# Kernel tuning notes

Hardware: AMD Instinct MI355X
Metric: run time of the kernel (lower is better)

The kernel has to match this reference:

```python
import jax, jax.numpy as jnp
import numpy as np

HIDDEN = 3072
N_HEADS = 24
N_KV = 8
HEAD_DIM = HIDDEN // N_HEADS          # 128
ROT = int(HEAD_DIM * 0.75)            # 96 (partial rotary)
OP_SIZE = N_HEADS * HEAD_DIM + 2 * N_KV * HEAD_DIM  # 5120
LORA_R = 256
LORA_SCALE = 512.0 / LORA_R           # 2.0
ROPE_THETA = 10000.0
SCALE = HEAD_DIM ** -0.5


def setup_inputs() -> dict:
    key = jax.random.key(0)
    ks = jax.random.split(key, 8)
    B, S = 2, 2048
    hidden_states = jax.random.normal(ks[0], (B, S, HIDDEN), dtype=jnp.float32)
    position_ids = jnp.arange(B * S, dtype=jnp.int64 if jax.config.jax_enable_x64 else jnp.int32).reshape(B, S)
    w = lambda k, o, i: jax.random.normal(k, (o, i), dtype=jnp.float32) * (i ** -0.5)
    return {
        "hidden_states": hidden_states,
        "Wqkv": w(ks[1], OP_SIZE, HIDDEN),
        "Aqkv": w(ks[2], LORA_R, HIDDEN),
        "Bqkv": w(ks[3], OP_SIZE, LORA_R) * 0.01,
        "Wo": w(ks[4], HIDDEN, N_HEADS * HEAD_DIM),
        "Ao": w(ks[5], LORA_R, N_HEADS * HEAD_DIM),
        "Bo": w(ks[6], HIDDEN, LORA_R) * 0.01,
        "position_ids": position_ids,
    }


def _lora_linear(x, W, A, Bm):
    # base GEMM + low-rank LoRA update, scaling = alpha/r
    return x @ W.T + (x @ A.T) @ Bm.T * LORA_SCALE


def _rotate_half(x):
    h = x.shape[-1] // 2
    return jnp.concatenate((-x[..., h:], x[..., :h]), axis=-1)


def reference(hidden_states, Wqkv, Aqkv, Bqkv, Wo, Ao, Bo, position_ids):
    B, S, _ = hidden_states.shape
    qkv = _lora_linear(hidden_states, Wqkv, Aqkv, Bqkv)  # [B,S,5120]
    q_pos = N_HEADS * HEAD_DIM
    kv_pos = N_KV * HEAD_DIM
    q = qkv[..., :q_pos].reshape(B, S, N_HEADS, HEAD_DIM)
    k = qkv[..., q_pos:q_pos + kv_pos].reshape(B, S, N_KV, HEAD_DIM)
    v = qkv[..., q_pos + kv_pos:].reshape(B, S, N_KV, HEAD_DIM)

    # partial RoPE: cos/sin cache over rotary_ndims=96
    inv_freq = 1.0 / (ROPE_THETA ** (jnp.arange(0, ROT, 2, dtype=jnp.float32) / ROT))  # [48]
    freqs = position_ids.astype(jnp.float32)[..., None] * inv_freq  # [B,S,48]
    emb = jnp.concatenate((freqs, freqs), axis=-1)                   # [B,S,96]
    cos = jnp.cos(emb)[:, :, None, :]  # broadcast over head axis (bsnd)
    sin = jnp.sin(emb)[:, :, None, :]

    def rope(x):
        xr, xp = x[..., :ROT], x[..., ROT:]
        xr = xr * cos + _rotate_half(xr) * sin
        return jnp.concatenate((xr, xp), axis=-1)

    q = rope(q)
    k = rope(k)

    # GQA: repeat kv heads to match query heads
    groups = N_HEADS // N_KV
    k = jnp.repeat(k, groups, axis=2)
    v = jnp.repeat(v, groups, axis=2)

    scores = jnp.einsum('bqhd,bkhd->bhqk', q, k) * SCALE  # [B,H,S,S]
    causal = jnp.tril(jnp.ones((S, S), dtype=bool))
    scores = jnp.where(causal, scores, jnp.finfo(scores.dtype).min)
    probs = jax.nn.softmax(scores, axis=-1)
    attn = jnp.einsum('bhqk,bkhd->bqhd', probs, v).reshape(B, S, N_HEADS * HEAD_DIM)
    return _lora_linear(attn, Wo, Ao, Bo)
```

## Files before the change

### kernel.cpp

```cpp
#include <hip/hip_runtime.h>

typedef unsigned short u16;
typedef unsigned int   u32;

typedef __bf16 bf16_t;
typedef bf16_t bf16x8 __attribute__((ext_vector_type(8)));
typedef float  f32x4  __attribute__((ext_vector_type(4)));
typedef float  f32x16 __attribute__((ext_vector_type(16)));
typedef u16    u16x8  __attribute__((ext_vector_type(8)));
typedef u32    u32x4  __attribute__((ext_vector_type(4)));

__device__ __forceinline__ float bf2f(u16 u) { return __uint_as_float(((u32)u) << 16); }
__device__ __forceinline__ u16 f2bf(float f) {
  u32 u = __float_as_uint(f);
  u32 r = u + 0x7fffu + ((u >> 16) & 1u);
  return (u16)(r >> 16);
}
__device__ __forceinline__ float fast_exp2(float x) { return __builtin_amdgcn_exp2f(x); }

__device__ __forceinline__ void gload_lds16(const u16* g, u16* l) {
  __builtin_amdgcn_global_load_lds(
      (const __attribute__((address_space(1))) void*)g,
      (__attribute__((address_space(3))) void*)l,
      16, 0, 0);
}

#define SBAR0() __builtin_amdgcn_sched_barrier(0)
#define HWBAR() __builtin_amdgcn_s_barrier()

__global__ void k_cast_str(const float* __restrict__ in, u16* __restrict__ out,
                           int C8, int L, int off, float scale) {
  const int r  = blockIdx.y;
  const int c8 = blockIdx.x * 128 + threadIdx.x;
  if (c8 >= C8) return;
  const f32x4* p = (const f32x4*)(in + (size_t)r * (C8 * 8) + c8 * 8);
  f32x4 a = p[0], b = p[1];
  u16x8 o;
  o[0] = f2bf(a[0] * scale); o[1] = f2bf(a[1] * scale);
  o[2] = f2bf(a[2] * scale); o[3] = f2bf(a[3] * scale);
  o[4] = f2bf(b[0] * scale); o[5] = f2bf(b[1] * scale);
  o[6] = f2bf(b[2] * scale); o[7] = f2bf(b[3] * scale);
  *(u16x8*)(out + (size_t)r * L + off + c8 * 8) = o;
}

__global__ void k_red4_cast(const float* __restrict__ t4, u16* __restrict__ out,
                            int C8, int L, int off, float scale, size_t plane) {
  const int r  = blockIdx.y;
  const int c8 = blockIdx.x * 64 + threadIdx.x;
  if (c8 >= C8) return;
  size_t base = (size_t)r * (C8 * 8) + c8 * 8;
  float s[8];
#pragma unroll
  for (int j = 0; j < 8; ++j) s[j] = 0.f;
#pragma unroll
  for (int p = 0; p < 4; ++p) {
    const f32x4* q = (const f32x4*)(t4 + p * plane + base);
    f32x4 a = q[0], b = q[1];
    s[0] += a[0]; s[1] += a[1]; s[2] += a[2]; s[3] += a[3];
    s[4] += b[0]; s[5] += b[1]; s[6] += b[2]; s[7] += b[3];
  }
  u16x8 o;
#pragma unroll
  for (int j = 0; j < 8; ++j) o[j] = f2bf(s[j] * scale);
  *(u16x8*)(out + (size_t)r * L + off + c8 * 8) = o;
}

__global__ __launch_bounds__(256) void k_gemm_bt_sk(
    const u16* __restrict__ A, const u16* __restrict__ B, float* __restrict__ C,
    int M, int N, int lda, int ldb, int kc) {
  __shared__ u16 As[64][64 + 8];
  __shared__ u16 Bs[64][64 + 8];
  const int tid   = threadIdx.x;
  const int lane  = tid & 63;
  const int w     = tid >> 6;
  const int wm    = (w >> 1) * 32;
  const int wn    = (w & 1) * 32;
  const int row16 = lane & 15;
  const int quad  = lane >> 4;
  const int m0 = blockIdx.y * 64;
  const int n0 = blockIdx.x * 64;
  const int ldr = tid >> 2;
  const int ldc = (tid & 3) * 16;
  const int z   = blockIdx.z;
  float* Cz = C + (size_t)z * M * N;
  const int kbeg = z * kc, kend = kbeg + kc;

  f32x4 acc[2][2] = {};

  for (int k0 = kbeg; k0 < kend; k0 += 64) {
    const u16* ga = A + (size_t)(m0 + ldr) * lda + (k0 + ldc);
    const u16* gb = B + (size_t)(n0 + ldr) * ldb + (k0 + ldc);
    u16x8 a0 = *(const u16x8*)ga;
    u16x8 a1 = *(const u16x8*)(ga + 8);
    u16x8 b0 = *(const u16x8*)gb;
    u16x8 b1 = *(const u16x8*)(gb + 8);
    __syncthreads();
    *(u16x8*)&As[ldr][ldc]     = a0;
    *(u16x8*)&As[ldr][ldc + 8] = a1;
    *(u16x8*)&Bs[ldr][ldc]     = b0;
    *(u16x8*)&Bs[ldr][ldc + 8] = b1;
    __syncthreads();
#pragma unroll
    for (int kk = 0; kk < 64; kk += 32) {
      bf16x8 af0 = *(const bf16x8*)&As[wm + row16][kk + quad * 8];
      bf16x8 af1 = *(const bf16x8*)&As[wm + 16 + row16][kk + quad * 8];
      bf16x8 bg0 = *(const bf16x8*)&Bs[wn + row16][kk + quad * 8];
      bf16x8 bg1 = *(const bf16x8*)&Bs[wn + 16 + row16][kk + quad * 8];
      acc[0][0] = __builtin_amdgcn_mfma_f32_16x16x32_bf16(af0, bg0, acc[0][0], 0, 0, 0);
      acc[0][1] = __builtin_amdgcn_mfma_f32_16x16x32_bf16(af0, bg1, acc[0][1], 0, 0, 0);
      acc[1][0] = __builtin_amdgcn_mfma_f32_16x16x32_bf16(af1, bg0, acc[1][0], 0, 0, 0);
      acc[1][1] = __builtin_amdgcn_mfma_f32_16x16x32_bf16(af1, bg1, acc[1][1], 0, 0, 0);
    }
  }
#pragma unroll
  for (int tm = 0; tm < 2; ++tm)
#pragma unroll
    for (int tn = 0; tn < 2; ++tn) {
      int gm = m0 + wm + tm * 16 + quad * 4;
      int gn = n0 + wn + tn * 16 + row16;
#pragma unroll
      for (int r = 0; r < 4; ++r)
        Cz[(size_t)(gm + r) * N + gn] = acc[tm][tn][r];
    }
}

__device__ __forceinline__ void stage_half(
    int H, int nt4,
    const u16* __restrict__ A, const u16* __restrict__ B, int K,
    int m0, int n0, u16* AsB, u16* BsB,
    int w, int rowin, int colsw) {
  if (H >= nt4) return;
  const int t = H >> 2, slot = H & 3;
  const int half = slot & 1;
  const u16* G = (slot < 2) ? A : B;
  const int r0 = (slot < 2) ? m0 : n0;
  u16* lds = ((slot < 2) ? AsB : BsB) + (t & 1) * 16384 + half * 8192;
  const int k0 = t * 64;
#pragma unroll
  for (int i = 0; i < 2; ++i) {
    const int chunk = w * 2 + i;
    const int row = half * 128 + chunk * 8 + rowin;
    gload_lds16(G + (size_t)(r0 + row) * K + k0 + colsw, lds + chunk * 512);
  }
}

__device__ __forceinline__ bf16x8 frag_ld(const u16* base, int row, int c16) {
  return *(const bf16x8*)(base + row * 64 + ((c16 ^ (row & 7)) << 3));
}

template <int RB>
__device__ __forceinline__ void gemm256_group(
    int k, int nt,
    const u16* __restrict__ A, const u16* __restrict__ B, int K,
    int m0, int n0, u16* AsB, u16* BsB,
    int wr, int wc, int row16, int quad, int w, int rowin, int colsw,
    f32x4 (&acc)[8][4]) {
  const u16* Ab = AsB + RB * 16384;
  const u16* Bb = BsB + RB * 16384;
  const int nt4 = nt * 4;
  bf16x8 a0[4][2], a1[4][2], b0[2][2], b1[2][2];

#pragma unroll
  for (int mf = 0; mf < 4; ++mf)
#pragma unroll
    for (int kk = 0; kk < 2; ++kk)
      a0[mf][kk] = frag_ld(Ab, wr * 128 + mf * 16 + row16, kk * 4 + quad);
#pragma unroll
  for (int nf = 0; nf < 2; ++nf)
#pragma unroll
    for (int kk = 0; kk < 2; ++kk)
      b0[nf][kk] = frag_ld(Bb, wc * 64 + nf * 16 + row16, kk * 4 + quad);
  stage_half(4 * k + 5, nt4, A, B, K, m0, n0, AsB, BsB, w, rowin, colsw);
  SBAR0(); HWBAR(); SBAR0();
  __builtin_amdgcn_s_setprio(1);
#pragma unroll
  for (int mf = 0; mf < 4; ++mf)
#pragma unroll
    for (int nf = 0; nf < 2; ++nf)
#pragma unroll
      for (int kk = 0; kk < 2; ++kk)
        acc[mf][nf] = __builtin_amdgcn_mfma_f32_16x16x32_bf16(a0[mf][kk], b0[nf][kk], acc[mf][nf], 0, 0, 0);
  __builtin_amdgcn_s_setprio(0);
  SBAR0(); HWBAR(); SBAR0();

#pragma unroll
  for (int nf = 0; nf < 2; ++nf)
#pragma unroll
    for (int kk = 0; kk < 2; ++kk)
      b1[nf][kk] = frag_ld(Bb, wc * 64 + 32 + nf * 16 + row16, kk * 4 + quad);
  stage_half(4 * k + 6, nt4, A, B, K, m0, n0, AsB, BsB, w, rowin, colsw);
  SBAR0(); HWBAR(); SBAR0();
  __builtin_amdgcn_s_setprio(1);
#pragma unroll
  for (int mf = 0; mf < 4; ++mf)
#pragma unroll
    for (int nf = 0; nf < 2; ++nf)
#pragma unroll
      for (int kk = 0; kk < 2; ++kk)
        acc[mf][2 + nf] = __builtin_amdgcn_mfma_f32_16x16x32_bf16(a0[mf][kk], b1[nf][kk], acc[mf][2 + nf], 0, 0, 0);
  __builtin_amdgcn_s_setprio(0);
  SBAR0(); HWBAR(); SBAR0();

#pragma unroll
  for (int mf = 0; mf < 4; ++mf)
#pragma unroll
    for (int kk = 0; kk < 2; ++kk)
      a1[mf][kk] = frag_ld(Ab, wr * 128 + 64 + mf * 16 + row16, kk * 4 + quad);
  stage_half(4 * k + 7, nt4, A, B, K, m0, n0, AsB, BsB, w, rowin, colsw);
  SBAR0(); HWBAR(); SBAR0();
  __builtin_amdgcn_s_setprio(1);
#pragma unroll
  for (int mf = 0; mf < 4; ++mf)
#pragma unroll
    for (int nf = 0; nf < 2; ++nf)
#pragma unroll
      for (int kk = 0; kk < 2; ++kk)
        acc[4 + mf][nf] = __builtin_amdgcn_mfma_f32_16x16x32_bf16(a1[mf][kk], b0[nf][kk], acc[4 + mf][nf], 0, 0, 0);
  __builtin_amdgcn_s_setprio(0);
  SBAR0(); HWBAR(); SBAR0();

  stage_half(4 * k + 8, nt4, A, B, K, m0, n0, AsB, BsB, w, rowin, colsw);
  SBAR0();
  if (k < nt - 2) { asm volatile("s_waitcnt vmcnt(2)" ::: "memory"); }
  else            { asm volatile("s_waitcnt vmcnt(0)" ::: "memory"); }
  HWBAR(); SBAR0();
  __builtin_amdgcn_s_setprio(1);
#pragma unroll
  for (int mf = 0; mf < 4; ++mf)
#pragma unroll
    for (int nf = 0; nf < 2; ++nf)
#pragma unroll
      for (int kk = 0; kk < 2; ++kk)
        acc[4 + mf][2 + nf] = __builtin_amdgcn_mfma_f32_16x16x32_bf16(a1[mf][kk], b1[nf][kk], acc[4 + mf][2 + nf], 0, 0, 0);
  __builtin_amdgcn_s_setprio(0);
  SBAR0(); HWBAR(); SBAR0();
}

__global__ __launch_bounds__(512, 2) void k_gemm256(
    const u16* __restrict__ A, const u16* __restrict__ B, float* __restrict__ C,
    int M, int N, int K) {
  __shared__ u16 As[2 * 16384];
  __shared__ u16 Bs[2 * 16384];

  const int tid   = threadIdx.x;
  const int lane  = tid & 63;
  const int w     = tid >> 6;
  const int wr    = w >> 2;
  const int wc    = w & 3;
  const int row16 = lane & 15;
  const int quad  = lane >> 4;
  const int rowin = lane >> 3;
  const int colsw = ((lane & 7) ^ (lane >> 3)) << 3;

  const int nwg = (int)gridDim.x;
  const int bid = (int)blockIdx.x;
  const int xcd = bid & 7, rest = bid >> 3;
  const int qq = nwg >> 3, rr = nwg & 7;
  const int wg = (xcd < rr ? xcd * (qq + 1) : rr * (qq + 1) + (xcd - rr) * qq) + rest;
  const int nbx = N >> 8;
  const int m0 = (wg / nbx) << 8;
  const int n0 = (wg % nbx) << 8;

  const int nt = K >> 6;
  f32x4 acc[8][4] = {};

#pragma unroll
  for (int H = 0; H < 5; ++H)
    stage_half(H, nt * 4, A, B, K, m0, n0, As, Bs, w, rowin, colsw);
  asm volatile("s_waitcnt vmcnt(2)" ::: "memory");
  HWBAR(); SBAR0();

  int k = 0;
  for (; k + 1 < nt; k += 2) {
    gemm256_group<0>(k,     nt, A, B, K, m0, n0, As, Bs, wr, wc, row16, quad, w, rowin, colsw, acc);
    gemm256_group<1>(k + 1, nt, A, B, K, m0, n0, As, Bs, wr, wc, row16, quad, w, rowin, colsw, acc);
  }
  if (k < nt)
    gemm256_group<0>(k, nt, A, B, K, m0, n0, As, Bs, wr, wc, row16, quad, w, rowin, colsw, acc);

#pragma unroll
  for (int mi = 0; mi < 8; ++mi) {
    const int gm = m0 + wr * 128 + mi * 16 + quad * 4;
#pragma unroll
    for (int nj = 0; nj < 4; ++nj) {
      const int gn = n0 + wc * 64 + nj * 16 + row16;
#pragma unroll
      for (int r = 0; r < 4; ++r)
        C[(size_t)(gm + r) * N + gn] = acc[mi][nj][r];
    }
  }
}

__global__ void k_rope_tab(const int* __restrict__ pos_ids, float* __restrict__ tab) {
  const int t = threadIdx.x;
  const int r = blockIdx.x * 4 + t / 48;
  const int j = t % 48;
  const float pos = (float)pos_ids[r];
  float invf = powf(10000.0f, -(float)j * (1.0f / 48.0f));
  float e = pos * invf;
  tab[(size_t)r * 96 + j]      = cosf(e);
  tab[(size_t)r * 96 + 48 + j] = sinf(e);
}

__global__ void k_rope_split(const float* __restrict__ qkv, const float* __restrict__ tab,
                             u16* __restrict__ qb, u16* __restrict__ kb) {
  const int r  = blockIdx.x;
  const int hh = blockIdx.y;
  const int d  = threadIdx.x;
  const float* src;
  if (hh < 24) src = qkv + (size_t)r * 5120 + hh * 128;
  else         src = qkv + (size_t)r * 5120 + 3072 + (hh - 24) * 128;
  float x = src[d];
  float outv;
  if (d >= 96) {
    outv = x;
  } else {
    int j = (d < 48) ? d : d - 48;
    float c  = tab[(size_t)r * 96 + j];
    float sn = tab[(size_t)r * 96 + 48 + j];
    if (d < 48) outv = x * c - src[d + 48] * sn;
    else        outv = x * c + src[d - 48] * sn;
  }
  u16 o = f2bf(outv);
  if (hh < 24) qb[((size_t)r * 24 + hh) * 128 + d] = o;
  else         kb[((size_t)r * 8 + (hh - 24)) * 128 + d] = o;
}

__global__ void k_vtrans(const float* __restrict__ qkv, u16* __restrict__ vtg) {
  const int d  = threadIdx.x;
  const int kg = blockIdx.x;
  const int bk = blockIdx.y;
  const int b = bk >> 3, kvh = bk & 7;
  const float* src = qkv + (size_t)(b * 2048 + kg * 8) * 5120 + 4096 + kvh * 128 + d;
  u16x8 pack;
#pragma unroll
  for (int t = 0; t < 8; ++t) pack[t] = f2bf(src[(size_t)t * 5120]);
  *(u16x8*)(vtg + ((size_t)bk * 128 + d) * 2048 + kg * 8) = pack;
}

__global__ __launch_bounds__(256) void k_attn_mfma(
    const u16* __restrict__ qb, const u16* __restrict__ kb, const u16* __restrict__ vtg,
    u16* __restrict__ attnw) {
  __shared__ u16 KsA[8192], VtA[8192], KsB[8192], VtB[8192];

  const int tid  = threadIdx.x;
  const int lane = tid & 63;
  const int w    = tid >> 6;
  const int l31  = lane & 31;
  const int hi   = lane >> 5;
  const int r7   = lane & 7;
  const int qt   = (int)gridDim.x - 1 - (int)blockIdx.x;
  const int bh   = blockIdx.y;
  const int b    = bh / 24;
  const int h    = bh % 24;
  const int kvh  = h / 3;
  const int q0   = qt * 128;
  const int qrow = q0 + w * 32 + l31;

  const u16* qrb = qb + (((size_t)(b * 2048 + qrow)) * 24 + h) * 128;
  bf16x8 qf[8];
#pragma unroll
  for (int kk = 0; kk < 8; ++kk) qf[kk] = *(const bf16x8*)(qrb + kk * 16 + hi * 8);

  const u16* kbbase = kb + ((size_t)(b * 2048) * 8 + kvh) * 128;
  const u16* vtbase = vtg + (size_t)(b * 8 + kvh) * 128 * 2048;

  f32x16 o32[4] = {};
  float m_st = -INFINITY, l_st = 0.f;
  const float C1 = 0.08838834764831845f * 1.4426950408889634f;
  const int ntile = 2 * qt + 2;

#define STAGE(Kd, Vd, KB0)                                                          \
  {                                                                                 \
    _Pragma("unroll")                                                               \
    for (int i = 0; i < 4; ++i) {                                                   \
      const int c = w * 4 + i;                                                      \
      const int rowk = 4 * c + (lane >> 4);                                         \
      gload_lds16(kbbase + (size_t)((KB0) + rowk) * 1024 +                          \
                      (((lane & 15) ^ (rowk & 7)) << 3),                            \
                  (Kd) + c * 512);                                                  \
      const int rowv = 8 * c + (lane >> 3);                                         \
      gload_lds16(vtbase + (size_t)rowv * 2048 + (KB0) +                            \
                      (((lane & 7) ^ (rowv & 7)) << 3),                             \
                  (Vd) + c * 512);                                                  \
    }                                                                               \
  }

  STAGE(KsA, VtA, 0);
  __syncthreads();

  for (int t = 0; t < ntile; ++t) {
    const int kb0 = t * 64;
    const u16* Kc = (t & 1) ? KsB : KsA;
    const u16* Vc = (t & 1) ? VtB : VtA;
    if (t + 1 < ntile) {
      u16* Kn = (t & 1) ? KsA : KsB;
      u16* Vn = (t & 1) ? VtA : VtB;
      STAGE(Kn, Vn, kb0 + 64);
    }

    f32x16 s[2] = {};
    __builtin_amdgcn_s_setprio(1);
#pragma unroll
    for (int kk = 0; kk < 8; ++kk) {
#pragma unroll
      for (int kt = 0; kt < 2; ++kt) {
        const int row = kt * 32 + l31;
        bf16x8 kf = *(const bf16x8*)&Kc[row * 128 + (((2 * kk + hi) ^ r7) << 3)];
        s[kt] = __builtin_amdgcn_mfma_f32_32x32x16_bf16(kf, qf[kk], s[kt], 0, 0, 0);
      }
    }
    __builtin_amdgcn_s_setprio(0);

    if (kb0 >= q0) {
#pragma unroll
      for (int kt = 0; kt < 2; ++kt)
#pragma unroll
        for (int r = 0; r < 16; ++r) {
          const int key = kb0 + 32 * kt + (r & 3) + 8 * (r >> 2) + 4 * hi;
          if (key > qrow) s[kt][r] = -INFINITY;
        }
    }

    float tm[16];
#pragma unroll
    for (int r = 0; r < 16; ++r) tm[r] = fmaxf(s[0][r], s[1][r]);
#pragma unroll
    for (int st = 8; st >= 1; st >>= 1)
#pragma unroll
      for (int r = 0; r < 8; ++r)
        if (r < st) tm[r] = fmaxf(tm[r], tm[r + st]);
    float mx = fmaxf(tm[0], __shfl_xor(tm[0], 32));

    const bool skip = __all((mx - m_st) * C1 <= 8.0f);
    if (!skip) {
      const float mnew = fmaxf(m_st, mx);
      const float alpha = fast_exp2((m_st - mnew) * C1);
      l_st *= alpha;
#pragma unroll
      for (int dt = 0; dt < 4; ++dt)
#pragma unroll
        for (int r = 0; r < 16; ++r) o32[dt][r] *= alpha;
      m_st = mnew;
    }
    const float mc = m_st * C1;
    float ts[16];
#pragma unroll
    for (int r = 0; r < 16; ++r) {
      float p0 = fast_exp2(__builtin_fmaf(s[0][r], C1, -mc));
      float p1 = fast_exp2(__builtin_fmaf(s[1][r], C1, -mc));
      s[0][r] = p0; s[1][r] = p1;
      ts[r] = p0 + p1;
    }
#pragma unroll
    for (int st = 8; st >= 1; st >>= 1)
#pragma unroll
      for (int r = 0; r < 8; ++r)
        if (r < st) ts[r] += ts[r + st];
    l_st += ts[0] + __shfl_xor(ts[0], 32);

    bf16x8 pb[4];
#pragma unroll
    for (int kt = 0; kt < 2; ++kt) {
      u32 pk[8];
#pragma unroll
      for (int i = 0; i < 8; ++i)
        asm("v_cvt_pk_bf16_f32 %0, %1, %2"
            : "=v"(pk[i]) : "v"(s[kt][2 * i]), "v"(s[kt][2 * i + 1]));
      u32 e0 = __shfl_xor(hi ? pk[0] : pk[2], 32);
      u32 e1 = __shfl_xor(hi ? pk[1] : pk[3], 32);
      u32 e2 = __shfl_xor(hi ? pk[4] : pk[6], 32);
      u32 e3 = __shfl_xor(hi ? pk[5] : pk[7], 32);
      u32x4 w0, w1;
      w0[0] = hi ? e0 : pk[0]; w0[1] = hi ? e1 : pk[1];
      w0[2] = hi ? pk[2] : e0; w0[3] = hi ? pk[3] : e1;
      w1[0] = hi ? e2 : pk[4]; w1[1] = hi ? e3 : pk[5];
      w1[2] = hi ? pk[6] : e2; w1[3] = hi ? pk[7] : e3;
      pb[2 * kt]     = __builtin_bit_cast(bf16x8, w0);
      pb[2 * kt + 1] = __builtin_bit_cast(bf16x8, w1);
    }

    __builtin_amdgcn_s_setprio(1);
#pragma unroll
    for (int ks = 0; ks < 4; ++ks) {
#pragma unroll
      for (int dt = 0; dt < 4; ++dt) {
        const int vrow = dt * 32 + l31;
        bf16x8 vf = *(const bf16x8*)&Vc[vrow * 64 + (((2 * ks + hi) ^ r7) << 3)];
        o32[dt] = __builtin_amdgcn_mfma_f32_32x32x16_bf16(vf, pb[ks], o32[dt], 0, 0, 0);
      }
    }
    __builtin_amdgcn_s_setprio(0);

    __syncthreads();
  }

  const float inv = 1.0f / l_st;
  u16* scr = ((w < 2) ? KsA : VtA) + (w & 1) * 4096;
#pragma unroll
  for (int dt = 0; dt < 4; ++dt)
#pragma unroll
    for (int r = 0; r < 16; ++r) {
      const int d = 32 * dt + (r & 3) + 8 * (r >> 2) + 4 * hi;
      const int slot = (d >> 3) ^ (l31 & 7);
      scr[l31 * 128 + slot * 8 + (d & 7)] = f2bf(o32[dt][r] * inv);
    }
  const int q32r = lane >> 1, part = lane & 1;
  const size_t grow = ((size_t)(b * 2048 + q0 + w * 32 + q32r)) * 3328 + (size_t)h * 128;
#pragma unroll
  for (int c = 0; c < 8; ++c) {
    const int d0 = part * 64 + c * 8;
    const int s2 = (d0 >> 3) ^ (q32r & 7);
    *(u16x8*)(attnw + grow + d0) = *(const u16x8*)&scr[q32r * 128 + s2 * 8];
  }
}

#define OFF_XW    ((size_t)0)
#define OFF_WWQ   ((size_t)27262976)
#define OFF_AQKVB ((size_t)61341696)
#define OFF_WWO   ((size_t)62914560)
#define OFF_AOB   ((size_t)83361792)
#define OFF_QKV   ((size_t)84934656)
#define OFF_TA    ((size_t)168820736)
#define OFF_TA4   OFF_QKV
#define OFF_QB    OFF_XW
#define OFF_KB    OFF_WWQ
#define OFF_VTG   (OFF_WWQ + (size_t)8388608)
#define OFF_RTAB  (OFF_WWQ + (size_t)16777216)
#define OFF_ATTNW OFF_QKV
#define OFF_TO4   (OFF_QKV + (size_t)27262976)

extern "C" void kernel_launch(void* const* d_in, const int* in_sizes, int n_in,
                              void* d_out, int out_size, void* d_ws, size_t ws_size,
                              hipStream_t stream) {
  const float* x    = (const float*)d_in[0];
  const float* Wqkv = (const float*)d_in[1];
  const float* Aqkv = (const float*)d_in[2];
  const float* Bqkv = (const float*)d_in[3];
  const float* Wo   = (const float*)d_in[4];
  const float* Ao   = (const float*)d_in[5];
  const float* Bo   = (const float*)d_in[6];
  const int*   pos  = (const int*)d_in[7];
  float* out = (float*)d_out;
  char* ws = (char*)d_ws;

  u16* xw    = (u16*)(ws + OFF_XW);
  u16* wwq   = (u16*)(ws + OFF_WWQ);
  u16* aqkvb = (u16*)(ws + OFF_AQKVB);
  u16* wwo   = (u16*)(ws + OFF_WWO);
  u16* aob   = (u16*)(ws + OFF_AOB);
  float* qkv = (float*)(ws + OFF_QKV);
  float* tA4 = (float*)(ws + OFF_TA4);
  u16* qb    = (u16*)(ws + OFF_QB);
  u16* kb    = (u16*)(ws + OFF_KB);
  u16* vtg   = (u16*)(ws + OFF_VTG);
  float* rtab = (float*)(ws + OFF_RTAB);
  u16* attnw = (u16*)(ws + OFF_ATTNW);
  float* tO4 = (float*)(ws + OFF_TO4);

  k_cast_str<<<dim3(3, 4096), 128, 0, stream>>>(x,    xw,  384, 3328, 0,    1.f);
  k_cast_str<<<dim3(3, 5120), 128, 0, stream>>>(Wqkv, wwq, 384, 3328, 0,    1.f);
  k_cast_str<<<dim3(1, 5120), 128, 0, stream>>>(Bqkv, wwq,  32, 3328, 3072, 1.f);
  k_cast_str<<<dim3(3, 256),  128, 0, stream>>>(Aqkv, aqkvb, 384, 3072, 0,  1.f);
  k_cast_str<<<dim3(3, 3072), 128, 0, stream>>>(Wo,   wwo, 384, 3328, 0,    1.f);
  k_cast_str<<<dim3(1, 3072), 128, 0, stream>>>(Bo,   wwo,  32, 3328, 3072, 1.f);
  k_cast_str<<<dim3(3, 256),  128, 0, stream>>>(Ao,   aob, 384, 3072, 0,    1.f);

  k_gemm_bt_sk<<<dim3(4, 64, 4), 256, 0, stream>>>(xw, aqkvb, tA4, 4096, 256, 3328, 3072, 768);
  k_red4_cast<<<dim3(1, 4096), 64, 0, stream>>>(tA4, xw, 32, 3328, 3072, 2.f, (size_t)4096 * 256);

  k_gemm256<<<dim3((5120 / 256) * (4096 / 256)), 512, 0, stream>>>(xw, wwq, qkv, 4096, 5120, 3328);

  k_rope_tab<<<dim3(1024), 192, 0, stream>>>(pos, rtab);
  k_rope_split<<<dim3(4096, 32), 128, 0, stream>>>(qkv, rtab, qb, kb);
  k_vtrans<<<dim3(256, 16), 128, 0, stream>>>(qkv, vtg);

  k_attn_mfma<<<dim3(16, 48), 256, 0, stream>>>(qb, kb, vtg, attnw);

  k_gemm_bt_sk<<<dim3(4, 64, 4), 256, 0, stream>>>(attnw, aob, tO4, 4096, 256, 3328, 3072, 768);
  k_red4_cast<<<dim3(1, 4096), 64, 0, stream>>>(tO4, attnw, 32, 3328, 3072, 2.f, (size_t)4096 * 256);

  k_gemm256<<<dim3((3072 / 256) * (4096 / 256)), 512, 0, stream>>>(attnw, wwo, out, 4096, 3072, 3328);
}
```

Baseline: 734.5 us.

## Merge cast and rope/vtrans launches, restructure attention staging for lower LDS

Replaces the seven separate fp32-to-bf16 cast launches with one grid-stride kernel, and merges the RoPE split and V transpose into one launch. These cut launch count and tail overhead. The attention kernel now keeps a single K buffer with double-buffered V. It loads Q fragments from global memory inside each tile instead of holding them in registers, and adds launch_bounds(256,4) so more blocks can be resident per CU. The trade-off is repeated Q global loads and extra barriers per tile, in exchange for lower LDS and register pressure.

```diff
diff --git a/kernel.cpp b/kernel.cpp
--- a/kernel.cpp
+++ b/kernel.cpp
@@ -28,19 +28,32 @@
 #define SBAR0() __builtin_amdgcn_sched_barrier(0)
 #define HWBAR() __builtin_amdgcn_s_barrier()
 
-__global__ void k_cast_str(const float* __restrict__ in, u16* __restrict__ out,
-                           int C8, int L, int off, float scale) {
-  const int r  = blockIdx.y;
-  const int c8 = blockIdx.x * 128 + threadIdx.x;
-  if (c8 >= C8) return;
-  const f32x4* p = (const f32x4*)(in + (size_t)r * (C8 * 8) + c8 * 8);
-  f32x4 a = p[0], b = p[1];
-  u16x8 o;
-  o[0] = f2bf(a[0] * scale); o[1] = f2bf(a[1] * scale);
-  o[2] = f2bf(a[2] * scale); o[3] = f2bf(a[3] * scale);
-  o[4] = f2bf(b[0] * scale); o[5] = f2bf(b[1] * scale);
-  o[6] = f2bf(b[2] * scale); o[7] = f2bf(b[3] * scale);
-  *(u16x8*)(out + (size_t)r * L + off + c8 * 8) = o;
+__global__ void k_cast_all(const float* __restrict__ x,  const float* __restrict__ wq,
+                           const float* __restrict__ bq, const float* __restrict__ aq,
+                           const float* __restrict__ wo, const float* __restrict__ bo,
+                           const float* __restrict__ ao,
+                           u16* __restrict__ xw, u16* __restrict__ wwq, u16* __restrict__ aqkvb,
+                           u16* __restrict__ wwo, u16* __restrict__ aob) {
+  const int total = 5177344;
+  int i = blockIdx.x * blockDim.x + threadIdx.x;
+  const int stride = gridDim.x * blockDim.x;
+  for (; i < total; i += stride) {
+    const float* src; u16* dst; int C8, L, off, loc;
+    if      (i < 1572864) { src = x;  dst = xw;    C8 = 384; L = 3328; off = 0;    loc = i; }
+    else if (i < 3538944) { src = wq; dst = wwq;   C8 = 384; L = 3328; off = 0;    loc = i - 1572864; }
+    else if (i < 3702784) { src = bq; dst = wwq;   C8 = 32;  L = 3328; off = 3072; loc = i - 3538944; }
+    else if (i < 3801088) { src = aq; dst = aqkvb; C8 = 384; L = 3072; off = 0;    loc = i - 3702784; }
+    else if (i < 4980736) { src = wo; dst = wwo;   C8 = 384; L = 3328; off = 0;    loc = i - 3801088; }
+    else if (i < 5079040) { src = bo; dst = wwo;   C8 = 32;  L = 3328; off = 3072; loc = i - 4980736; }
+    else                  { src = ao; dst = aob;   C8 = 384; L = 3072; off = 0;    loc = i - 5079040; }
+    const int r = loc / C8, c8 = loc - r * C8;
+    const f32x4* p = (const f32x4*)(src + ((size_t)r * C8 + c8) * 8);
+    f32x4 a = p[0], b2 = p[1];
+    u16x8 o;
+    o[0] = f2bf(a[0]);  o[1] = f2bf(a[1]);  o[2] = f2bf(a[2]);  o[3] = f2bf(a[3]);
+    o[4] = f2bf(b2[0]); o[5] = f2bf(b2[1]); o[6] = f2bf(b2[2]); o[7] = f2bf(b2[3]);
+    *(u16x8*)(dst + (size_t)r * L + off + c8 * 8) = o;
+  }
 }
 
 __global__ void k_red4_cast(const float* __restrict__ t4, u16* __restrict__ out,
@@ -302,46 +315,47 @@
   tab[(size_t)r * 96 + 48 + j] = sinf(e);
 }
 
-__global__ void k_rope_split(const float* __restrict__ qkv, const float* __restrict__ tab,
-                             u16* __restrict__ qb, u16* __restrict__ kb) {
-  const int r  = blockIdx.x;
-  const int hh = blockIdx.y;
-  const int d  = threadIdx.x;
-  const float* src;
-  if (hh < 24) src = qkv + (size_t)r * 5120 + hh * 128;
-  else         src = qkv + (size_t)r * 5120 + 3072 + (hh - 24) * 128;
-  float x = src[d];
-  float outv;
-  if (d >= 96) {
-    outv = x;
+__global__ void k_rope_v(const float* __restrict__ qkv, const float* __restrict__ tab,
+                         u16* __restrict__ qb, u16* __restrict__ kb, u16* __restrict__ vtg) {
+  const int y = blockIdx.y;
+  const int d = threadIdx.x;
+  if (y < 32) {
+    const int r  = blockIdx.x;
+    const int hh = y;
+    const float* src;
+    if (hh < 24) src = qkv + (size_t)r * 5120 + hh * 128;
+    else         src = qkv + (size_t)r * 5120 + 3072 + (hh - 24) * 128;
+    float x = src[d];
+    float outv;
+    if (d >= 96) {
+      outv = x;
+    } else {
+      int j = (d < 48) ? d : d - 48;
+      float c  = tab[(size_t)r * 96 + j];
+      float sn = tab[(size_t)r * 96 + 48 + j];
+      if (d < 48) outv = x * c - src[d + 48] * sn;
+      else        outv = x * c + src[d - 48] * sn;
+    }
+    u16 o = f2bf(outv);
+    if (hh < 24) qb[((size_t)r * 24 + hh) * 128 + d] = o;
+    else         kb[((size_t)r * 8 + (hh - 24)) * 128 + d] = o;
   } else {
-    int j = (d < 48) ? d : d - 48;
-    float c  = tab[(size_t)r * 96 + j];
-    float sn = tab[(size_t)r * 96 + 48 + j];
-    if (d < 48) outv = x * c - src[d + 48] * sn;
-    else        outv = x * c + src[d - 48] * sn;
-  }
-  u16 o = f2bf(outv);
-  if (hh < 24) qb[((size_t)r * 24 + hh) * 128 + d] = o;
-  else         kb[((size_t)r * 8 + (hh - 24)) * 128 + d] = o;
-}
-
-__global__ void k_vtrans(const float* __restrict__ qkv, u16* __restrict__ vtg) {
-  const int d  = threadIdx.x;
-  const int kg = blockIdx.x;
-  const int bk = blockIdx.y;
-  const int b = bk >> 3, kvh = bk & 7;
-  const float* src = qkv + (size_t)(b * 2048 + kg * 8) * 5120 + 4096 + kvh * 128 + d;
-  u16x8 pack;
-#pragma unroll
-  for (int t = 0; t < 8; ++t) pack[t] = f2bf(src[(size_t)t * 5120]);
-  *(u16x8*)(vtg + ((size_t)bk * 128 + d) * 2048 + kg * 8) = pack;
-}
-
-__global__ __launch_bounds__(256) void k_attn_mfma(
+    const int bk = blockIdx.x >> 8;
+    const int kg = blockIdx.x & 255;
+    const int b = bk >> 3, kvh = bk & 7;
+    const float* src = qkv + (size_t)(b * 2048 + kg * 8) * 5120 + 4096 + kvh * 128 + d;
+    u16x8 pack;
+#pragma unroll
+    for (int t = 0; t < 8; ++t) pack[t] = f2bf(src[(size_t)t * 5120]);
+    *(u16x8*)(vtg + ((size_t)bk * 128 + d) * 2048 + kg * 8) = pack;
+  }
+}
+
+__global__ __launch_bounds__(256, 4) void k_attn_mfma(
     const u16* __restrict__ qb, const u16* __restrict__ kb, const u16* __restrict__ vtg,
     u16* __restrict__ attnw) {
-  __shared__ u16 KsA[8192], VtA[8192], KsB[8192], VtB[8192];
+  __shared__ u16 Ks[8192];
+  __shared__ u16 Vt[2][8192];
 
   const int tid  = threadIdx.x;
   const int lane = tid & 63;
@@ -357,11 +371,7 @@
   const int q0   = qt * 128;
   const int qrow = q0 + w * 32 + l31;
 
-  const u16* qrb = qb + (((size_t)(b * 2048 + qrow)) * 24 + h) * 128;
-  bf16x8 qf[8];
-#pragma unroll
-  for (int kk = 0; kk < 8; ++kk) qf[kk] = *(const bf16x8*)(qrb + kk * 16 + hi * 8);
-
+  const u16* qrb    = qb + (((size_t)(b * 2048 + qrow)) * 24 + h) * 128;
   const u16* kbbase = kb + ((size_t)(b * 2048) * 8 + kvh) * 128;
   const u16* vtbase = vtg + (size_t)(b * 8 + kvh) * 128 * 2048;
 
@@ -370,65 +380,80 @@
   const float C1 = 0.08838834764831845f * 1.4426950408889634f;
   const int ntile = 2 * qt + 2;
 
-#define STAGE(Kd, Vd, KB0)                                                          \
-  {                                                                                 \
-    _Pragma("unroll")                                                               \
-    for (int i = 0; i < 4; ++i) {                                                   \
-      const int c = w * 4 + i;                                                      \
-      const int rowk = 4 * c + (lane >> 4);                                         \
-      gload_lds16(kbbase + (size_t)((KB0) + rowk) * 1024 +                          \
-                      (((lane & 15) ^ (rowk & 7)) << 3),                            \
-                  (Kd) + c * 512);                                                  \
-      const int rowv = 8 * c + (lane >> 3);                                         \
-      gload_lds16(vtbase + (size_t)rowv * 2048 + (KB0) +                            \
-                      (((lane & 7) ^ (rowv & 7)) << 3),                             \
-                  (Vd) + c * 512);                                                  \
-    }                                                                               \
-  }
-
-  STAGE(KsA, VtA, 0);
-  __syncthreads();
+#define STAGE_K(KB0)                                                            \
+  { _Pragma("unroll") for (int i = 0; i < 4; ++i) {                             \
+      const int c = w * 4 + i;                                                  \
+      const int rowk = 4 * c + (lane >> 4);                                     \
+      gload_lds16(kbbase + (size_t)((KB0) + rowk) * 1024 +                      \
+                      (((lane & 15) ^ (rowk & 7)) << 3),                        \
+                  Ks + c * 512); } }
+#define STAGE_V(Vd, KB0)                                                        \
+  { _Pragma("unroll") for (int i = 0; i < 4; ++i) {                             \
+      const int c = w * 4 + i;                                                  \
+      const int rowv = 8 * c + (lane >> 3);                                     \
+      gload_lds16(vtbase + (size_t)rowv * 2048 + (KB0) +                        \
+                      (((lane & 7) ^ (rowv & 7)) << 3),                         \
+                  (Vd) + c * 512); } }
+
+  STAGE_K(0);
+  STAGE_V(Vt[0], 0);
+  asm volatile("s_waitcnt vmcnt(0)" ::: "memory");
+  SBAR0(); HWBAR(); SBAR0();
 
   for (int t = 0; t < ntile; ++t) {
     const int kb0 = t * 64;
-    const u16* Kc = (t & 1) ? KsB : KsA;
-    const u16* Vc = (t & 1) ? VtB : VtA;
-    if (t + 1 < ntile) {
-      u16* Kn = (t & 1) ? KsA : KsB;
-      u16* Vn = (t & 1) ? VtA : VtB;
-      STAGE(Kn, Vn, kb0 + 64);
-    }
-
-    f32x16 s[2] = {};
-    __builtin_amdgcn_s_setprio(1);
-#pragma unroll
-    for (int kk = 0; kk < 8; ++kk) {
-#pragma unroll
-      for (int kt = 0; kt < 2; ++kt) {
-        const int row = kt * 32 + l31;
-        bf16x8 kf = *(const bf16x8*)&Kc[row * 128 + (((2 * kk + hi) ^ r7) << 3)];
-        s[kt] = __builtin_amdgcn_mfma_f32_32x32x16_bf16(kf, qf[kk], s[kt], 0, 0, 0);
+    const u16* Vc = Vt[t & 1];
+    if (t + 1 < ntile) STAGE_V(Vt[(t + 1) & 1], kb0 + 64);
+    SBAR0();
+
+    f32x16 s0 = {}, s1 = {};
+    {
+      bf16x8 qa[4];
+#pragma unroll
+      for (int kk = 0; kk < 4; ++kk) qa[kk] = *(const bf16x8*)(qrb + kk * 16 + hi * 8);
+      __builtin_amdgcn_s_setprio(1);
+#pragma unroll
+      for (int kk = 0; kk < 4; ++kk) {
+        bf16x8 kf0 = *(const bf16x8*)&Ks[l31 * 128 + (((2 * kk + hi) ^ r7) << 3)];
+        s0 = __builtin_amdgcn_mfma_f32_32x32x16_bf16(kf0, qa[kk], s0, 0, 0, 0);
+        bf16x8 kf1 = *(const bf16x8*)&Ks[(32 + l31) * 128 + (((2 * kk + hi) ^ ((32 + l31) & 7)) << 3)];
+        s1 = __builtin_amdgcn_mfma_f32_32x32x16_bf16(kf1, qa[kk], s1, 0, 0, 0);
       }
-    }
-    __builtin_amdgcn_s_setprio(0);
+      __builtin_amdgcn_s_setprio(0);
+#pragma unroll
+      for (int kk = 0; kk < 4; ++kk) qa[kk] = *(const bf16x8*)(qrb + 64 + kk * 16 + hi * 8);
+      __builtin_amdgcn_s_setprio(1);
+#pragma unroll
+      for (int kk = 4; kk < 8; ++kk) {
+        bf16x8 kf0 = *(const bf16x8*)&Ks[l31 * 128 + (((2 * kk + hi) ^ r7) << 3)];
+        s0 = __builtin_amdgcn_mfma_f32_32x32x16_bf16(kf0, qa[kk - 4], s0, 0, 0, 0);
+        bf16x8 kf1 = *(const bf16x8*)&Ks[(32 + l31) * 128 + (((2 * kk + hi) ^ ((32 + l31) & 7)) << 3)];
+        s1 = __builtin_amdgcn_mfma_f32_32x32x16_bf16(kf1, qa[kk - 4], s1, 0, 0, 0);
+      }
+      __builtin_amdgcn_s_setprio(0);
+    }
+
+    SBAR0(); HWBAR(); SBAR0();
+    if (t + 1 < ntile) STAGE_K(kb0 + 64);
+    SBAR0();
 
     if (kb0 >= q0) {
 #pragma unroll
-      for (int kt = 0; kt < 2; ++kt)
-#pragma unroll
-        for (int r = 0; r < 16; ++r) {
-          const int key = kb0 + 32 * kt + (r & 3) + 8 * (r >> 2) + 4 * hi;
-          if (key > qrow) s[kt][r] = -INFINITY;
-        }
-    }
-
-    float tm[16];
-#pragma unroll
-    for (int r = 0; r < 16; ++r) tm[r] = fmaxf(s[0][r], s[1][r]);
-#pragma unroll
-    for (int st = 8; st >= 1; st >>= 1)
-#pragma unroll
-      for (int r = 0; r < 8; ++r)
+      for (int r = 0; r < 16; ++r) {
+        const int crow = (r & 3) + 8 * (r >> 2) + 4 * hi;
+        if (kb0 + crow > qrow)      s0[r] = -INFINITY;
+        if (kb0 + 32 + crow > qrow) s1[r] = -INFINITY;
+      }
+    }
+
+    float tm[8];
+#pragma unroll
+    for (int r = 0; r < 8; ++r)
+      tm[r] = fmaxf(fmaxf(s0[r], s0[r + 8]), fmaxf(s1[r], s1[r + 8]));
+#pragma unroll
+    for (int st = 4; st >= 1; st >>= 1)
+#pragma unroll
+      for (int r = 0; r < 4; ++r)
         if (r < st) tm[r] = fmaxf(tm[r], tm[r + st]);
     float mx = fmaxf(tm[0], __shfl_xor(tm[0], 32));
 
@@ -444,29 +469,29 @@
       m_st = mnew;
     }
     const float mc = m_st * C1;
-    float ts[16];
+    float ts[8];
 #pragma unroll
     for (int r = 0; r < 16; ++r) {
-      float p0 = fast_exp2(__builtin_fmaf(s[0][r], C1, -mc));
-      float p1 = fast_exp2(__builtin_fmaf(s[1][r], C1, -mc));
-      s[0][r] = p0; s[1][r] = p1;
-      ts[r] = p0 + p1;
-    }
-#pragma unroll
-    for (int st = 8; st >= 1; st >>= 1)
-#pragma unroll
-      for (int r = 0; r < 8; ++r)
+      s0[r] = fast_exp2(__builtin_fmaf(s0[r], C1, -mc));
+      s1[r] = fast_exp2(__builtin_fmaf(s1[r], C1, -mc));
+    }
+#pragma unroll
+    for (int r = 0; r < 8; ++r) ts[r] = (s0[r] + s0[r + 8]) + (s1[r] + s1[r + 8]);
+#pragma unroll
+    for (int st = 4; st >= 1; st >>= 1)
+#pragma unroll
+      for (int r = 0; r < 4; ++r)
         if (r < st) ts[r] += ts[r + st];
     l_st += ts[0] + __shfl_xor(ts[0], 32);
 
-    bf16x8 pb[4];
 #pragma unroll
     for (int kt = 0; kt < 2; ++kt) {
+      const f32x16& sv = kt ? s1 : s0;
       u32 pk[8];
 #pragma unroll
       for (int i = 0; i < 8; ++i)
         asm("v_cvt_pk_bf16_f32 %0, %1, %2"
-            : "=v"(pk[i]) : "v"(s[kt][2 * i]), "v"(s[kt][2 * i + 1]));
+            : "=v"(pk[i]) : "v"(sv[2 * i]), "v"(sv[2 * i + 1]));
       u32 e0 = __shfl_xor(hi ? pk[0] : pk[2], 32);
       u32 e1 = __shfl_xor(hi ? pk[1] : pk[3], 32);
       u32 e2 = __shfl_xor(hi ? pk[4] : pk[6], 32);
@@ -476,27 +501,26 @@
       w0[2] = hi ? pk[2] : e0; w0[3] = hi ? pk[3] : e1;
       w1[0] = hi ? e2 : pk[4]; w1[1] = hi ? e3 : pk[5];
       w1[2] = hi ? pk[6] : e2; w1[3] = hi ? pk[7] : e3;
-      pb[2 * kt]     = __builtin_bit_cast(bf16x8, w0);
-      pb[2 * kt + 1] = __builtin_bit_cast(bf16x8, w1);
-    }
-
-    __builtin_amdgcn_s_setprio(1);
-#pragma unroll
-    for (int ks = 0; ks < 4; ++ks) {
+      bf16x8 pb0 = __builtin_bit_cast(bf16x8, w0);
+      bf16x8 pb1 = __builtin_bit_cast(bf16x8, w1);
+      __builtin_amdgcn_s_setprio(1);
 #pragma unroll
       for (int dt = 0; dt < 4; ++dt) {
         const int vrow = dt * 32 + l31;
-        bf16x8 vf = *(const bf16x8*)&Vc[vrow * 64 + (((2 * ks + hi) ^ r7) << 3)];
-        o32[dt] = __builtin_amdgcn_mfma_f32_32x32x16_bf16(vf, pb[ks], o32[dt], 0, 0, 0);
+        bf16x8 vf0 = *(const bf16x8*)&Vc[vrow * 64 + (((2 * (2 * kt) + hi) ^ (vrow & 7)) << 3)];
+        o32[dt] = __builtin_amdgcn_mfma_f32_32x32x16_bf16(vf0, pb0, o32[dt], 0, 0, 0);
+        bf16x8 vf1 = *(const bf16x8*)&Vc[vrow * 64 + (((2 * (2 * kt + 1) + hi) ^ (vrow & 7)) << 3)];
+        o32[dt] = __builtin_amdgcn_mfma_f32_32x32x16_bf16(vf1, pb1, o32[dt], 0, 0, 0);
       }
-    }
-    __builtin_amdgcn_s_setprio(0);
-
-    __syncthreads();
+      __builtin_amdgcn_s_setprio(0);
+    }
+
+    asm volatile("s_waitcnt vmcnt(0)" ::: "memory");
+    SBAR0(); HWBAR(); SBAR0();
   }
 
   const float inv = 1.0f / l_st;
-  u16* scr = ((w < 2) ? KsA : VtA) + (w & 1) * 4096;
+  u16* scr = Vt[w >> 1] + (w & 1) * 4096;
 #pragma unroll
   for (int dt = 0; dt < 4; ++dt)
 #pragma unroll
@@ -521,7 +545,6 @@
 #define OFF_WWO   ((size_t)62914560)
 #define OFF_AOB   ((size_t)83361792)
 #define OFF_QKV   ((size_t)84934656)
-#define OFF_TA    ((size_t)168820736)
 #define OFF_TA4   OFF_QKV
 #define OFF_QB    OFF_XW
 #define OFF_KB    OFF_WWQ
@@ -558,13 +581,8 @@
   u16* attnw = (u16*)(ws + OFF_ATTNW);
   float* tO4 = (float*)(ws + OFF_TO4);
 
-  k_cast_str<<<dim3(3, 4096), 128, 0, stream>>>(x,    xw,  384, 3328, 0,    1.f);
-  k_cast_str<<<dim3(3, 5120), 128, 0, stream>>>(Wqkv, wwq, 384, 3328, 0,    1.f);
-  k_cast_str<<<dim3(1, 5120), 128, 0, stream>>>(Bqkv, wwq,  32, 3328, 3072, 1.f);
-  k_cast_str<<<dim3(3, 256),  128, 0, stream>>>(Aqkv, aqkvb, 384, 3072, 0,  1.f);
-  k_cast_str<<<dim3(3, 3072), 128, 0, stream>>>(Wo,   wwo, 384, 3328, 0,    1.f);
-  k_cast_str<<<dim3(1, 3072), 128, 0, stream>>>(Bo,   wwo,  32, 3328, 3072, 1.f);
-  k_cast_str<<<dim3(3, 256),  128, 0, stream>>>(Ao,   aob, 384, 3072, 0,    1.f);
+  k_cast_all<<<2048, 256, 0, stream>>>(x, Wqkv, Bqkv, Aqkv, Wo, Bo, Ao,
+                                       xw, wwq, aqkvb, wwo, aob);
 
   k_gemm_bt_sk<<<dim3(4, 64, 4), 256, 0, stream>>>(xw, aqkvb, tA4, 4096, 256, 3328, 3072, 768);
   k_red4_cast<<<dim3(1, 4096), 64, 0, stream>>>(tA4, xw, 32, 3328, 3072, 2.f, (size_t)4096 * 256);
@@ -572,8 +590,7 @@
   k_gemm256<<<dim3((5120 / 256) * (4096 / 256)), 512, 0, stream>>>(xw, wwq, qkv, 4096, 5120, 3328);
 
   k_rope_tab<<<dim3(1024), 192, 0, stream>>>(pos, rtab);
-  k_rope_split<<<dim3(4096, 32), 128, 0, stream>>>(qkv, rtab, qb, kb);
-  k_vtrans<<<dim3(256, 16), 128, 0, stream>>>(qkv, vtg);
+  k_rope_v<<<dim3(4096, 33), 128, 0, stream>>>(qkv, rtab, qb, kb, vtg);
 
   k_attn_mfma<<<dim3(16, 48), 256, 0, stream>>>(qb, kb, vtg, attnw);
 
```

Result: no change. 744.4 us (+1.4%).
